# Kernel tuning notes

Hardware: AMD Instinct MI355X
Metric: run time of the kernel (lower is better)

Reference implementation:

```python
import jax, jax.numpy as jnp
import numpy as np
import math

N_HEAD = 16
D_K = 64
D_V = 64


def setup_inputs() -> dict:
    key = jax.random.key(0)
    ks = jax.random.split(key, 6)
    B, N, D = 32, 4096, 1024
    scale = 0.02
    return {
        "query": jax.random.normal(ks[0], (B, D), dtype=jnp.float32),
        "key": jax.random.normal(ks[1], (B, N, D), dtype=jnp.float32),
        "value": jax.random.normal(ks[2], (B, N, D), dtype=jnp.float32),
        "wq": jax.random.normal(ks[3], (D, N_HEAD * D_K), dtype=jnp.float32) * scale,
        "wk": jax.random.normal(ks[4], (D, N_HEAD * D_K), dtype=jnp.float32) * scale,
        "wv": jax.random.normal(ks[5], (D, N_HEAD * D_V), dtype=jnp.float32) * scale,
    }


def reference(query, key, value, wq, wk, wv):
    B = query.shape[0]
    N = key.shape[1]
    # projections (weights stored [in, out], equivalent to torch x @ W.T)
    q = (query @ wq).reshape(B, N_HEAD, D_K)            # [B, H, dk] (seq_len1 == 1)
    k = (key @ wk).reshape(B, N, N_HEAD, D_K)           # [B, N, H, dk]
    v = (value @ wv).reshape(B, N, N_HEAD, D_V)         # [B, N, H, dv]
    scores = jnp.einsum("bhd,bnhd->bhn", q, k) / math.sqrt(D_K)  # [B, H, N]
    attn = jax.nn.softmax(scores, axis=-1)
    out = jnp.einsum("bhn,bnhd->bhd", attn, v)          # [B, H, dv]
    return out.reshape(B, N_HEAD * D_V)
```

## Files before the change

### kernel.cpp

```cpp
#include <hip/hip_runtime.h>
#include <hip/hip_bf16.h>

#define B_SZ 32
#define NSEQ 4096
#define DM   1024
#define NH   16

typedef __attribute__((ext_vector_type(8))) short bf16x8;
typedef __attribute__((ext_vector_type(4))) float f32x4;

__device__ __forceinline__ short f2bf(float f) {
  unsigned int x = __float_as_uint(f);
  unsigned int r = (x + 0x7fffu + ((x >> 16) & 1u)) >> 16;
  return (short)r;
}

__global__ __launch_bounds__(64) void qw_kernel(
    const float* __restrict__ query, const float* __restrict__ wq,
    const float* __restrict__ wk, short* __restrict__ qw16) {
  int b = blockIdx.x >> 4, h = blockIdx.x & 15;
  int t = threadIdx.x;
  __shared__ float qs[DM];
  __shared__ float qh[64];
  const f32x4* q4 = (const f32x4*)(query + (size_t)b * DM);
  f32x4* qs4 = (f32x4*)qs;
  for (int i = t; i < DM / 4; i += 64) qs4[i] = q4[i];
  __syncthreads();
  float acc = 0.f;
  const float* wqc = wq + h * 64 + t;
  #pragma unroll 8
  for (int D = 0; D < DM; ++D) acc += qs[D] * wqc[(size_t)D * DM];
  qh[t] = acc * 0.125f;
  __syncthreads();
  for (int k = 0; k < 16; ++k) {
    int D = t + 64 * k;
    const f32x4* wk4 = (const f32x4*)(wk + (size_t)D * DM + h * 64);
    float a = 0.f;
    #pragma unroll
    for (int j = 0; j < 16; ++j) {
      f32x4 w = wk4[j];
      a += qh[j * 4 + 0] * w[0] + qh[j * 4 + 1] * w[1] +
           qh[j * 4 + 2] * w[2] + qh[j * 4 + 3] * w[3];
    }
    qw16[((size_t)b * NH + h) * DM + D] = f2bf(a);
  }
}

__global__ __launch_bounds__(256) void scores_kernel(
    const float* __restrict__ key, const short* __restrict__ qw16,
    float* __restrict__ scores) {
  int blk = blockIdx.x;
  int b  = blk >> 6;
  int ng = blk & 63;
  int wave = threadIdx.x >> 6;
  int lane = threadIdx.x & 63;
  int quad = lane >> 4;
  int lm   = lane & 15;
  int n0 = ng * 64 + wave * 16;
  const float* ka = key  + ((size_t)b * NSEQ + n0 + lm) * DM + quad * 8;
  const short* bb = qw16 + ((size_t)b * NH   + lm) * DM + quad * 8;
  f32x4 acc = {0.f, 0.f, 0.f, 0.f};
  #pragma unroll 4
  for (int kc = 0; kc < 32; ++kc) {
    f32x4 a0 = *(const f32x4*)(ka + kc * 32);
    f32x4 a1 = *(const f32x4*)(ka + kc * 32 + 4);
    bf16x8 bfrag = *(const bf16x8*)(bb + kc * 32);
    bf16x8 afrag;
    afrag[0] = f2bf(a0[0]); afrag[1] = f2bf(a0[1]);
    afrag[2] = f2bf(a0[2]); afrag[3] = f2bf(a0[3]);
    afrag[4] = f2bf(a1[0]); afrag[5] = f2bf(a1[1]);
    afrag[6] = f2bf(a1[2]); afrag[7] = f2bf(a1[3]);
    acc = __builtin_amdgcn_mfma_f32_16x16x32_bf16(afrag, bfrag, acc, 0, 0, 0);
  }
  size_t sidx = ((size_t)b * NH + lm) * NSEQ + n0 + quad * 4;
  *(f32x4*)(scores + sidx) = acc;
}

__global__ __launch_bounds__(256) void softmax_kernel(
    const float* __restrict__ scores, short* __restrict__ P) {
  int bh = blockIdx.x;
  int t = threadIdx.x;
  int lane = t & 63, wave = t >> 6;
  const f32x4* row = (const f32x4*)(scores + (size_t)bh * NSEQ);
  f32x4 v[4];
  float m = -1e30f;
  #pragma unroll
  for (int i = 0; i < 4; ++i) {
    v[i] = row[t + 256 * i];
    m = fmaxf(m, fmaxf(fmaxf(v[i][0], v[i][1]), fmaxf(v[i][2], v[i][3])));
  }
  #pragma unroll
  for (int off = 32; off > 0; off >>= 1) m = fmaxf(m, __shfl_xor(m, off));
  __shared__ float sm[4], ss[4];
  if (lane == 0) sm[wave] = m;
  __syncthreads();
  m = fmaxf(fmaxf(sm[0], sm[1]), fmaxf(sm[2], sm[3]));
  float s = 0.f;
  #pragma unroll
  for (int i = 0; i < 4; ++i)
    #pragma unroll
    for (int j = 0; j < 4; ++j) { v[i][j] = __expf(v[i][j] - m); s += v[i][j]; }
  #pragma unroll
  for (int off = 32; off > 0; off >>= 1) s += __shfl_xor(s, off);
  if (lane == 0) ss[wave] = s;
  __syncthreads();
  float inv = 1.f / (ss[0] + ss[1] + ss[2] + ss[3]);
  short* Pr = P + (size_t)bh * NSEQ;
  #pragma unroll
  for (int i = 0; i < 4; ++i) {
    short4 p;
    p.x = f2bf(v[i][0] * inv); p.y = f2bf(v[i][1] * inv);
    p.z = f2bf(v[i][2] * inv); p.w = f2bf(v[i][3] * inv);
    *(short4*)(Pr + (size_t)(t + 256 * i) * 4) = p;
  }
}

__global__ __launch_bounds__(256) void ctx_kernel(
    const float* __restrict__ value, const short* __restrict__ P,
    float* __restrict__ ctxp) {
  int blk = blockIdx.x;
  int ns = blk & 3;
  int Dg = (blk >> 2) & 15;
  int b  = blk >> 6;
  int wave = threadIdx.x >> 6, lane = threadIdx.x & 63;
  int quad = lane >> 4, lm = lane & 15;
  int col = Dg * 64 + wave * 16 + lm;
  int n0 = ns * 1024;
  const short* pa = P + ((size_t)b * NH + lm) * NSEQ + n0 + quad * 8;
  const float* vb = value + ((size_t)b * NSEQ + n0 + quad * 8) * DM + col;
  f32x4 acc = {0.f, 0.f, 0.f, 0.f};
  #pragma unroll 2
  for (int kc = 0; kc < 32; ++kc) {
    bf16x8 afrag = *(const bf16x8*)(pa + kc * 32);
    const float* vp = vb + (size_t)kc * 32 * DM;
    bf16x8 bfrag;
    #pragma unroll
    for (int j = 0; j < 8; ++j) bfrag[j] = f2bf(vp[(size_t)j * DM]);
    acc = __builtin_amdgcn_mfma_f32_16x16x32_bf16(afrag, bfrag, acc, 0, 0, 0);
  }
  #pragma unroll
  for (int r = 0; r < 4; ++r) {
    int h = quad * 4 + r;
    ctxp[(((size_t)ns * B_SZ + b) * NH + h) * DM + col] = acc[r];
  }
}

__global__ __launch_bounds__(256) void out_kernel(
    const float* __restrict__ ctxp, const float* __restrict__ wv,
    float* __restrict__ out) {
  int b = blockIdx.x >> 4, h = blockIdx.x & 15;
  int t = threadIdx.x;
  __shared__ float ctx[DM];
  for (int i = t; i < DM; i += 256) {
    float s = 0.f;
    #pragma unroll
    for (int ns = 0; ns < 4; ++ns)
      s += ctxp[(((size_t)ns * B_SZ + b) * NH + h) * DM + i];
    ctx[i] = s;
  }
  __syncthreads();
  int d = t & 63, q = t >> 6;
  float acc = 0.f;
  #pragma unroll 4
  for (int D = q * 256; D < (q + 1) * 256; ++D)
    acc += ctx[D] * wv[(size_t)D * DM + h * 64 + d];
  __shared__ float red[256];
  red[t] = acc;
  __syncthreads();
  if (t < 64)
    out[(size_t)b * DM + h * 64 + t] =
        red[t] + red[t + 64] + red[t + 128] + red[t + 192];
}

extern "C" void kernel_launch(void* const* d_in, const int* in_sizes, int n_in,
                              void* d_out, int out_size, void* d_ws, size_t ws_size,
                              hipStream_t stream) {
  const float* query = (const float*)d_in[0];
  const float* key   = (const float*)d_in[1];
  const float* value = (const float*)d_in[2];
  const float* wq    = (const float*)d_in[3];
  const float* wk    = (const float*)d_in[4];
  const float* wv    = (const float*)d_in[5];
  float* out = (float*)d_out;
  char* ws = (char*)d_ws;

  short* qw16   = (short*)(ws);
  float* scores = (float*)(ws + (1u << 20));
  short* P      = (short*)(ws + (9u << 20));
  float* ctxp   = (float*)(ws + (13u << 20));

  qw_kernel     <<<B_SZ * NH, 64,  0, stream>>>(query, wq, wk, qw16);
  scores_kernel <<<B_SZ * 64, 256, 0, stream>>>(key, qw16, scores);
  softmax_kernel<<<B_SZ * NH, 256, 0, stream>>>(scores, P);
  ctx_kernel    <<<B_SZ * 64, 256, 0, stream>>>(value, P, ctxp);
  out_kernel    <<<B_SZ * NH, 256, 0, stream>>>(ctxp, wv, out);
}
```

Baseline: 1.159 ms.

## Stage key/value tiles through LDS with coalesced loads; widen qw kernel

The scores and ctx kernels now load fp32 key/value rows with coalesced 16-byte loads, convert them to bf16 once into padded shared-memory tiles, and read MFMA fragments from LDS. This replaces the strided per-lane global loads, above all the column-strided value gathers in ctx_kernel. ctx_kernel now computes a 256-column slice per block with four accumulators and launches fewer blocks. qw_kernel moves from 64 to 256 threads and splits the Wq reduction across waves. The cost is extra barriers and shared-memory traffic, and the ctx grid shrinks to 512 blocks, which may cut occupancy.

Result: faster. 1.114 ms (-3.8%).

```diff
diff --git a/kernel.cpp b/kernel.cpp
--- a/kernel.cpp
+++ b/kernel.cpp
@@ -1,12 +1,13 @@
 #include <hip/hip_runtime.h>
-#include <hip/hip_bf16.h>
 
 #define B_SZ 32
 #define NSEQ 4096
 #define DM   1024
 #define NH   16
+#define NS   4
 
 typedef __attribute__((ext_vector_type(8))) short bf16x8;
+typedef __attribute__((ext_vector_type(4))) short s16x4;
 typedef __attribute__((ext_vector_type(4))) float f32x4;
 
 __device__ __forceinline__ short f2bf(float f) {
@@ -15,25 +16,31 @@
   return (short)r;
 }
 
-__global__ __launch_bounds__(64) void qw_kernel(
+__global__ __launch_bounds__(256) void qw_kernel(
     const float* __restrict__ query, const float* __restrict__ wq,
     const float* __restrict__ wk, short* __restrict__ qw16) {
   int b = blockIdx.x >> 4, h = blockIdx.x & 15;
   int t = threadIdx.x;
   __shared__ float qs[DM];
+  __shared__ float red[256];
   __shared__ float qh[64];
-  const f32x4* q4 = (const f32x4*)(query + (size_t)b * DM);
-  f32x4* qs4 = (f32x4*)qs;
-  for (int i = t; i < DM / 4; i += 64) qs4[i] = q4[i];
-  __syncthreads();
-  float acc = 0.f;
-  const float* wqc = wq + h * 64 + t;
-  #pragma unroll 8
-  for (int D = 0; D < DM; ++D) acc += qs[D] * wqc[(size_t)D * DM];
-  qh[t] = acc * 0.125f;
-  __syncthreads();
-  for (int k = 0; k < 16; ++k) {
-    int D = t + 64 * k;
+  ((f32x4*)qs)[t] = ((const f32x4*)(query + (size_t)b * DM))[t];
+  __syncthreads();
+  int q = t >> 6, d = t & 63;
+  {
+    const float* wqc = wq + h * 64 + d;
+    float acc = 0.f;
+    #pragma unroll 8
+    for (int D = q * 256; D < q * 256 + 256; ++D)
+      acc += qs[D] * wqc[(size_t)D * DM];
+    red[t] = acc;
+  }
+  __syncthreads();
+  if (t < 64)
+    qh[t] = (red[t] + red[t + 64] + red[t + 128] + red[t + 192]) * 0.125f;
+  __syncthreads();
+  for (int k = 0; k < 4; ++k) {
+    int D = t + 256 * k;
     const f32x4* wk4 = (const f32x4*)(wk + (size_t)D * DM + h * 64);
     float a = 0.f;
     #pragma unroll
@@ -50,29 +57,34 @@
     const float* __restrict__ key, const short* __restrict__ qw16,
     float* __restrict__ scores) {
   int blk = blockIdx.x;
-  int b  = blk >> 6;
-  int ng = blk & 63;
-  int wave = threadIdx.x >> 6;
-  int lane = threadIdx.x & 63;
-  int quad = lane >> 4;
-  int lm   = lane & 15;
-  int n0 = ng * 64 + wave * 16;
-  const float* ka = key  + ((size_t)b * NSEQ + n0 + lm) * DM + quad * 8;
-  const short* bb = qw16 + ((size_t)b * NH   + lm) * DM + quad * 8;
+  int b = blk >> 6, ng = blk & 63;
+  int n0 = ng * 64;
+  int t = threadIdx.x;
+  int wave = t >> 6, lane = t & 63, quad = lane >> 4, lm = lane & 15;
+  __shared__ short kt[64][264];
+  const float* kbase = key + ((size_t)b * NSEQ + n0) * DM;
+  const short* bb = qw16 + ((size_t)b * NH + lm) * DM + quad * 8;
   f32x4 acc = {0.f, 0.f, 0.f, 0.f};
-  #pragma unroll 4
-  for (int kc = 0; kc < 32; ++kc) {
-    f32x4 a0 = *(const f32x4*)(ka + kc * 32);
-    f32x4 a1 = *(const f32x4*)(ka + kc * 32 + 4);
-    bf16x8 bfrag = *(const bf16x8*)(bb + kc * 32);
-    bf16x8 afrag;
-    afrag[0] = f2bf(a0[0]); afrag[1] = f2bf(a0[1]);
-    afrag[2] = f2bf(a0[2]); afrag[3] = f2bf(a0[3]);
-    afrag[4] = f2bf(a1[0]); afrag[5] = f2bf(a1[1]);
-    afrag[6] = f2bf(a1[2]); afrag[7] = f2bf(a1[3]);
-    acc = __builtin_amdgcn_mfma_f32_16x16x32_bf16(afrag, bfrag, acc, 0, 0, 0);
-  }
-  size_t sidx = ((size_t)b * NH + lm) * NSEQ + n0 + quad * 4;
+  for (int kch = 0; kch < 4; ++kch) {
+    #pragma unroll
+    for (int i = 0; i < 16; ++i) {
+      int r = i * 4 + wave;
+      f32x4 v = *(const f32x4*)(kbase + (size_t)r * DM + kch * 256 + lane * 4);
+      s16x4 p;
+      p[0] = f2bf(v[0]); p[1] = f2bf(v[1]);
+      p[2] = f2bf(v[2]); p[3] = f2bf(v[3]);
+      *(s16x4*)&kt[r][lane * 4] = p;
+    }
+    __syncthreads();
+    #pragma unroll
+    for (int kc = 0; kc < 8; ++kc) {
+      bf16x8 afrag = *(const bf16x8*)&kt[wave * 16 + lm][kc * 32 + quad * 8];
+      bf16x8 bfrag = *(const bf16x8*)(bb + kch * 256 + kc * 32);
+      acc = __builtin_amdgcn_mfma_f32_16x16x32_bf16(afrag, bfrag, acc, 0, 0, 0);
+    }
+    __syncthreads();
+  }
+  size_t sidx = ((size_t)b * NH + lm) * NSEQ + n0 + wave * 16 + quad * 4;
   *(f32x4*)(scores + sidx) = acc;
 }
 
@@ -119,29 +131,48 @@
     const float* __restrict__ value, const short* __restrict__ P,
     float* __restrict__ ctxp) {
   int blk = blockIdx.x;
+  int b  = blk >> 4;
+  int Dg = (blk >> 2) & 3;
   int ns = blk & 3;
-  int Dg = (blk >> 2) & 15;
-  int b  = blk >> 6;
-  int wave = threadIdx.x >> 6, lane = threadIdx.x & 63;
-  int quad = lane >> 4, lm = lane & 15;
-  int col = Dg * 64 + wave * 16 + lm;
-  int n0 = ns * 1024;
-  const short* pa = P + ((size_t)b * NH + lm) * NSEQ + n0 + quad * 8;
-  const float* vb = value + ((size_t)b * NSEQ + n0 + quad * 8) * DM + col;
-  f32x4 acc = {0.f, 0.f, 0.f, 0.f};
-  #pragma unroll 2
-  for (int kc = 0; kc < 32; ++kc) {
-    bf16x8 afrag = *(const bf16x8*)(pa + kc * 32);
-    const float* vp = vb + (size_t)kc * 32 * DM;
-    bf16x8 bfrag;
-    #pragma unroll
-    for (int j = 0; j < 8; ++j) bfrag[j] = f2bf(vp[(size_t)j * DM]);
-    acc = __builtin_amdgcn_mfma_f32_16x16x32_bf16(afrag, bfrag, acc, 0, 0, 0);
-  }
-  #pragma unroll
-  for (int r = 0; r < 4; ++r) {
-    int h = quad * 4 + r;
-    ctxp[(((size_t)ns * B_SZ + b) * NH + h) * DM + col] = acc[r];
+  int t = threadIdx.x;
+  int wave = t >> 6, lane = t & 63, quad = lane >> 4, lm = lane & 15;
+  __shared__ short vt[32][260];
+  const float* vbase = value + ((size_t)b * NSEQ + ns * 1024) * DM + Dg * 256;
+  const short* pbase = P + ((size_t)b * NH + lm) * NSEQ + ns * 1024 + quad * 8;
+  f32x4 acc[4];
+  #pragma unroll
+  for (int i = 0; i < 4; ++i) acc[i] = (f32x4){0.f, 0.f, 0.f, 0.f};
+  for (int nc = 0; nc < 32; ++nc) {
+    const float* src = vbase + (size_t)(nc * 32 + wave) * DM + lane * 4;
+    #pragma unroll
+    for (int i = 0; i < 8; ++i) {
+      f32x4 v = *(const f32x4*)(src + (size_t)(i * 4) * DM);
+      s16x4 p;
+      p[0] = f2bf(v[0]); p[1] = f2bf(v[1]);
+      p[2] = f2bf(v[2]); p[3] = f2bf(v[3]);
+      *(s16x4*)&vt[wave + i * 4][lane * 4] = p;
+    }
+    __syncthreads();
+    bf16x8 pfrag = *(const bf16x8*)(pbase + nc * 32);
+    #pragma unroll
+    for (int dt = 0; dt < 4; ++dt) {
+      int cb = wave * 64 + dt * 16 + lm;
+      bf16x8 bfrag;
+      #pragma unroll
+      for (int j = 0; j < 8; ++j)
+        bfrag[j] = vt[quad * 8 + j][cb];
+      acc[dt] = __builtin_amdgcn_mfma_f32_16x16x32_bf16(pfrag, bfrag, acc[dt], 0, 0, 0);
+    }
+    __syncthreads();
+  }
+  #pragma unroll
+  for (int dt = 0; dt < 4; ++dt) {
+    int Dc = Dg * 256 + wave * 64 + dt * 16 + lm;
+    #pragma unroll
+    for (int r = 0; r < 4; ++r) {
+      int h = quad * 4 + r;
+      ctxp[(((size_t)ns * B_SZ + b) * NH + h) * DM + Dc] = acc[dt][r];
+    }
   }
 }
 
@@ -154,7 +185,7 @@
   for (int i = t; i < DM; i += 256) {
     float s = 0.f;
     #pragma unroll
-    for (int ns = 0; ns < 4; ++ns)
+    for (int ns = 0; ns < NS; ++ns)
       s += ctxp[(((size_t)ns * B_SZ + b) * NH + h) * DM + i];
     ctx[i] = s;
   }
@@ -189,9 +220,9 @@
   short* P      = (short*)(ws + (9u << 20));
   float* ctxp   = (float*)(ws + (13u << 20));
 
-  qw_kernel     <<<B_SZ * NH, 64,  0, stream>>>(query, wq, wk, qw16);
+  qw_kernel     <<<B_SZ * NH, 256, 0, stream>>>(query, wq, wk, qw16);
   scores_kernel <<<B_SZ * 64, 256, 0, stream>>>(key, qw16, scores);
   softmax_kernel<<<B_SZ * NH, 256, 0, stream>>>(scores, P);
-  ctx_kernel    <<<B_SZ * 64, 256, 0, stream>>>(value, P, ctxp);
+  ctx_kernel    <<<B_SZ * 16, 256, 0, stream>>>(value, P, ctxp);
   out_kernel    <<<B_SZ * NH, 256, 0, stream>>>(ctxp, wv, out);
 }
```
